# Optimization experiments

Measured on AMD Instinct MI355X. Metric: run time of the kernel, lower is better.

## Reference

```python
import jax, jax.numpy as jnp
import numpy as np

N, E, F_IN, D, H, G, T = 30000, 480000, 128, 32, 4, 128, 10
HD = H * D
NEG_SLOPE = 0.2


def _lin(key, fan_out, fan_in, scale=0.05):
    k1, k2 = jax.random.split(key)
    return (jax.random.normal(k1, (fan_out, fan_in), jnp.float32) * scale,
            jax.random.normal(k2, (fan_out,), jnp.float32) * scale)


def setup_inputs() -> dict:
    key = jax.random.key(0)
    ks = jax.random.split(key, 24)
    x = jax.random.normal(ks[0], (N, F_IN), jnp.float32)
    edge_index = jax.random.randint(ks[1], (2, E), 0, N, jnp.int64)
    batch = jnp.sort(jax.random.randint(ks[2], (N,), 0, G, jnp.int64))
    inp = {"x": x, "edge_index": edge_index, "batch": batch}
    # conv 0 (in=F_IN) and conv 1 (in=D); each followed by Linear(HD -> D)
    for i, fin in enumerate([F_IN, D]):
        base = 3 + i * 8
        Wl, bl = _lin(ks[base + 0], HD, fin)
        Wr, br = _lin(ks[base + 1], HD, fin)
        att = jax.random.normal(ks[base + 2], (H, D), jnp.float32) * 0.05
        bias = jnp.zeros((HD,), jnp.float32)
        lw, lb = _lin(ks[base + 3], D, HD)
        inp.update({f"Wl{i}": Wl, f"bl{i}": bl, f"Wr{i}": Wr, f"br{i}": br,
                    f"att{i}": att, f"cb{i}": bias, f"lw{i}": lw, f"lb{i}": lb})
    inp["fc1_W"], inp["fc1_b"] = _lin(ks[20], D, D)
    inp["fc2_W"], inp["fc2_b"] = _lin(ks[21], T, D)
    return inp


def _gatv2_conv(x, src, dst, Wl, bl, Wr, br, att, bias):
    # PyG GATv2Conv, concat=True, add_self_loops already applied to src/dst,
    # aggr='mean', eval mode (no dropout).
    n = x.shape[0]
    xl = (x @ Wl.T + bl).reshape(n, H, D)
    xr = (x @ Wr.T + br).reshape(n, H, D)
    e = jax.nn.leaky_relu(xl[src] + xr[dst], NEG_SLOPE)          # [E', H, D]
    alpha = jnp.einsum('ehd,hd->eh', e, att)                      # [E', H]
    amax = jax.ops.segment_max(alpha, dst, num_segments=n)        # [n, H]
    ex = jnp.exp(alpha - amax[dst])
    denom = jax.ops.segment_sum(ex, dst, num_segments=n)
    a = ex / denom[dst]                                           # softmax per target
    msg = xl[src] * a[:, :, None]                                 # [E', H, D]
    s = jax.ops.segment_sum(msg, dst, num_segments=n)
    cnt = jax.ops.segment_sum(jnp.ones((src.shape[0],), jnp.float32), dst, num_segments=n)
    out = s / cnt[:, None, None]                                  # mean aggregation
    return out.reshape(n, HD) + bias


def reference(x, edge_index, batch,
              Wl0, bl0, Wr0, br0, att0, cb0, lw0, lb0,
              Wl1, bl1, Wr1, br1, att1, cb1, lw1, lb1,
              fc1_W, fc1_b, fc2_W, fc2_b):
    loop = jnp.arange(N, dtype=edge_index.dtype)
    src = jnp.concatenate([edge_index[0], loop])  # add self loops
    dst = jnp.concatenate([edge_index[1], loop])
    convs = [(Wl0, bl0, Wr0, br0, att0, cb0, lw0, lb0),
             (Wl1, bl1, Wr1, br1, att1, cb1, lw1, lb1)]
    h = x
    for (Wl, bl, Wr, br, att, cb, lw, lb) in convs:
        h = _gatv2_conv(h, src, dst, Wl, bl, Wr, br, att, cb)
        h = h @ lw.T + lb  # heads>1: Linear(H*D -> D)
    g = jax.ops.segment_max(h, batch, num_segments=G)  # global max pool
    g = jax.nn.relu(g @ fc1_W.T + fc1_b)
    return g @ fc2_W.T + fc2_b
```

## Files before the change

### kernel.cpp

```cpp
#include <hip/hip_runtime.h>
#include <hip/hip_bf16.h>
#include <hip/hip_fp16.h>

#define NEG_SLOPE 0.2f
#define GGRP 128
#define TOUT 10

__global__ void init_kernel(int* __restrict__ deg, float* __restrict__ gpool,
                            int* __restrict__ csr_pad, int n, int gsize) {
    int i = blockIdx.x * blockDim.x + threadIdx.x;
    if (i < n) deg[i] = 0;
    if (i < gsize) gpool[i] = -__builtin_inff();
    if (i < 64) csr_pad[i] = 0;
}

__global__ void degree_kernel(const int* __restrict__ dst, int* __restrict__ deg, int E) {
    int i = blockIdx.x * blockDim.x + threadIdx.x;
    int base = i * 4;
    if (base + 3 < E) {
        int4 d = *(const int4*)(dst + base);
        atomicAdd(&deg[d.x], 1); atomicAdd(&deg[d.y], 1);
        atomicAdd(&deg[d.z], 1); atomicAdd(&deg[d.w], 1);
    } else {
        for (int k = base; k < E; ++k) atomicAdd(&deg[dst[k]], 1);
    }
}

__global__ __launch_bounds__(256)
void scanA_kernel(const int* __restrict__ deg, int* __restrict__ rowptr,
                  int* __restrict__ bsum, int n) {
    __shared__ int wsum[4];
    int tid = threadIdx.x, lane = tid & 63, wid = tid >> 6;
    int idx = blockIdx.x * 256 + tid;
    int v = (idx < n) ? deg[idx] : 0;
    int x = v;
    #pragma unroll
    for (int off = 1; off < 64; off <<= 1) {
        int t = __shfl_up(x, off, 64);
        if (lane >= off) x += t;
    }
    if (lane == 63) wsum[wid] = x;
    __syncthreads();
    if (tid == 0) {
        int s = 0;
        #pragma unroll
        for (int i = 0; i < 4; ++i) { int t = wsum[i]; wsum[i] = s; s += t; }
        bsum[blockIdx.x] = s;
    }
    __syncthreads();
    int excl = x - v + wsum[wid];
    if (idx < n) rowptr[idx] = excl;
}

__global__ __launch_bounds__(256)
void scanC_kernel(int* __restrict__ rowptr, int* __restrict__ cursor,
                  const int* __restrict__ bsum, int n, int nb) {
    __shared__ int soff_sh;
    int tid = threadIdx.x;
    int bx = blockIdx.x;
    if (tid < 64) {
        int lane = tid;
        int v = 0;
        if (lane < nb && lane < bx) v = bsum[lane];
        if (lane + 64 < nb && lane + 64 < bx) v += bsum[lane + 64];
        #pragma unroll
        for (int off = 32; off >= 1; off >>= 1) v += __shfl_xor(v, off, 64);
        if (lane == 0) soff_sh = v;
        if (bx == 0) {
            int t = 0;
            if (lane < nb) t = bsum[lane];
            if (lane + 64 < nb) t += bsum[lane + 64];
            #pragma unroll
            for (int off = 32; off >= 1; off >>= 1) t += __shfl_xor(t, off, 64);
            if (lane == 0) rowptr[n] = t;
        }
    }
    __syncthreads();
    int idx = bx * 256 + tid;
    if (idx < n) {
        int r = rowptr[idx] + soff_sh;
        rowptr[idx] = r;
        cursor[idx] = r;
    }
}

__global__ void scatter_kernel(const int* __restrict__ src, const int* __restrict__ dst,
                               int* __restrict__ cursor, int* __restrict__ csr, int E) {
    int i = blockIdx.x * blockDim.x + threadIdx.x;
    int base = i * 4;
    if (base + 3 < E) {
        int4 s = *(const int4*)(src + base);
        int4 d = *(const int4*)(dst + base);
        csr[atomicAdd(&cursor[d.x], 1)] = s.x << 8;
        csr[atomicAdd(&cursor[d.y], 1)] = s.y << 8;
        csr[atomicAdd(&cursor[d.z], 1)] = s.z << 8;
        csr[atomicAdd(&cursor[d.w], 1)] = s.w << 8;
    } else {
        for (int k = base; k < E; ++k)
            csr[atomicAdd(&cursor[dst[k]], 1)] = src[k] << 8;
    }
}

template <int FIN>
__global__ __launch_bounds__(256, 2)
void gemm_tile_kernel(const float* __restrict__ X,
                      const float* __restrict__ Wl, const float* __restrict__ bl,
                      const float* __restrict__ Wr, const float* __restrict__ br,
                      float* __restrict__ xl, float* __restrict__ xr,
                      __half* __restrict__ xlh,
                      int n, int nRowBlk) {
    constexpr int BK = 32, BM = 128, LDA = BM + 4;
    constexpr int NCHUNK = FIN / BK;
    __shared__ float Xs[BK][LDA];
    __shared__ float Ws[BK][LDA];
    int tid = threadIdx.x;
    int rowBlk = blockIdx.x;
    int colBlk = 0;
    if (rowBlk >= nRowBlk) { rowBlk -= nRowBlk; colBlk = 1; }
    const float* __restrict__ Wb = colBlk ? Wr : Wl;
    const float* __restrict__ bb = colBlk ? br : bl;
    float* __restrict__ ob = colBlk ? xr : xl;
    int row0 = rowBlk * BM;

    int sr  = tid >> 3;
    int skq = (tid & 7) * 4;

    float4 xpre[4], wpre[4];

    auto load_pre = [&](int c) {
        int k0 = c * BK;
        #pragma unroll
        for (int i = 0; i < 4; ++i) {
            int r = sr + i * 32;
            int gr = row0 + r;
            float4 v = {0.f, 0.f, 0.f, 0.f};
            if (gr < n) v = *(const float4*)&X[(size_t)gr * FIN + k0 + skq];
            xpre[i] = v;
            wpre[i] = *(const float4*)&Wb[(size_t)r * FIN + k0 + skq];
        }
    };
    auto store_pre = [&]() {
        #pragma unroll
        for (int i = 0; i < 4; ++i) {
            int r = sr + i * 32;
            Xs[skq + 0][r] = xpre[i].x; Xs[skq + 1][r] = xpre[i].y;
            Xs[skq + 2][r] = xpre[i].z; Xs[skq + 3][r] = xpre[i].w;
            Ws[skq + 0][r] = wpre[i].x; Ws[skq + 1][r] = wpre[i].y;
            Ws[skq + 2][r] = wpre[i].z; Ws[skq + 3][r] = wpre[i].w;
        }
    };

    load_pre(0);
    store_pre();
    __syncthreads();

    int tx = tid & 15;
    int ty = tid >> 4;
    float acc[8][8];
    #pragma unroll
    for (int i = 0; i < 8; ++i)
        #pragma unroll
        for (int j = 0; j < 8; ++j) acc[i][j] = 0.f;

    #pragma unroll
    for (int c = 0; c < NCHUNK; ++c) {
        if (c + 1 < NCHUNK) load_pre(c + 1);
        #pragma unroll 8
        for (int k = 0; k < BK; ++k) {
            float4 a0 = *(const float4*)&Xs[k][ty * 8];
            float4 a1 = *(const float4*)&Xs[k][ty * 8 + 4];
            float4 b0 = *(const float4*)&Ws[k][tx * 8];
            float4 b1 = *(const float4*)&Ws[k][tx * 8 + 4];
            float av[8] = {a0.x, a0.y, a0.z, a0.w, a1.x, a1.y, a1.z, a1.w};
            float bv[8] = {b0.x, b0.y, b0.z, b0.w, b1.x, b1.y, b1.z, b1.w};
            #pragma unroll
            for (int i = 0; i < 8; ++i)
                #pragma unroll
                for (int j = 0; j < 8; ++j)
                    acc[i][j] = fmaf(av[i], bv[j], acc[i][j]);
        }
        if (c + 1 < NCHUNK) {
            __syncthreads();
            store_pre();
            __syncthreads();
        }
    }

    float bias[8];
    #pragma unroll
    for (int j = 0; j < 8; ++j) bias[j] = bb[tx * 8 + j];
    #pragma unroll
    for (int i = 0; i < 8; ++i) {
        int gr = row0 + ty * 8 + i;
        if (gr < n) {
            float v[8];
            #pragma unroll
            for (int j = 0; j < 8; ++j) v[j] = acc[i][j] + bias[j];
            float4 o0 = {v[0], v[1], v[2], v[3]};
            float4 o1 = {v[4], v[5], v[6], v[7]};
            *(float4*)&ob[(size_t)gr * 128 + tx * 8]     = o0;
            *(float4*)&ob[(size_t)gr * 128 + tx * 8 + 4] = o1;
            if (colBlk == 0) {
                union { __half2 h2[4]; uint4 u; } pk;
                #pragma unroll
                for (int j = 0; j < 4; ++j)
                    pk.h2[j] = __halves2half2(__float2half_rn(v[2 * j]),
                                              __float2half_rn(v[2 * j + 1]));
                *(uint4*)&xlh[(size_t)gr * 128 + tx * 8] = pk.u;
            }
        }
    }
}

__global__ __launch_bounds__(256)
void gat_fused_kernel(const float* __restrict__ xl, const __half* __restrict__ xlh,
                      const float* __restrict__ xr,
                      const float* __restrict__ att, const float* __restrict__ cb,
                      const float* __restrict__ lw, const float* __restrict__ lb,
                      const int* __restrict__ rowptr, const int* __restrict__ csrb,
                      float* __restrict__ out , int n) {
    __shared__ float lws[32][132];
    __shared__ float oslot[4][128];
    int tid = threadIdx.x;
    #pragma unroll
    for (int i = 0; i < 16; ++i) {
        int idx = tid + i * 256;
        lws[idx >> 7][idx & 127] = lw[idx];
    }
    __syncthreads();

    int wid = tid >> 6, lane = tid & 63;
    int nd = blockIdx.x * 4 + wid;
    if (nd >= n) return;
    int q4  = lane >> 4;
    int l16 = lane & 15;
    int fb  = l16 * 32;
    int fbh = l16 * 16;

    const char* __restrict__ xlb  = (const char*)xl;
    const char* __restrict__ xlhb = (const char*)xlh;
    const char* __restrict__ xrb  = (const char*)xr;
    int selfoff = nd << 9;

    const float4 xrA  = *(const float4*)(xrb + selfoff + fb);
    const float4 xrB  = *(const float4*)(xrb + selfoff + fb + 16);
    const float4 atA  = *(const float4*)((const char*)att + fb);
    const float4 atB  = *(const float4*)((const char*)att + fb + 16);
    const float4 xlsA = *(const float4*)(xlb + selfoff + fb);
    const float4 xlsB = *(const float4*)(xlb + selfoff + fb + 16);

    int start = rowptr[nd], end = rowptr[nd + 1];
    float cnt = (float)(end - start + 1);

    float den;
    float accA[4], accB[4];

    {
        float e0 = xlsA.x + xrA.x; e0 = fmaf(NEG_SLOPE, fminf(e0, 0.f), fmaxf(e0, 0.f));
        float e1 = xlsA.y + xrA.y; e1 = fmaf(NEG_SLOPE, fminf(e1, 0.f), fmaxf(e1, 0.f));
        float e2 = xlsA.z + xrA.z; e2 = fmaf(NEG_SLOPE, fminf(e2, 0.f), fmaxf(e2, 0.f));
        float e3 = xlsA.w + xrA.w; e3 = fmaf(NEG_SLOPE, fminf(e3, 0.f), fmaxf(e3, 0.f));
        float e4 = xlsB.x + xrB.x; e4 = fmaf(NEG_SLOPE, fminf(e4, 0.f), fmaxf(e4, 0.f));
        float e5 = xlsB.y + xrB.y; e5 = fmaf(NEG_SLOPE, fminf(e5, 0.f), fmaxf(e5, 0.f));
        float e6 = xlsB.z + xrB.z; e6 = fmaf(NEG_SLOPE, fminf(e6, 0.f), fmaxf(e6, 0.f));
        float e7 = xlsB.w + xrB.w; e7 = fmaf(NEG_SLOPE, fminf(e7, 0.f), fmaxf(e7, 0.f));
        float q = e0 * atA.x + e1 * atA.y + e2 * atA.z + e3 * atA.w
                + e4 * atB.x + e5 * atB.y + e6 * atB.z + e7 * atB.w;
        q += __shfl_xor(q, 1); q += __shfl_xor(q, 2);
        float a = __expf(q);
        if (q4 == 0) {
            den = a;
            accA[0] = a * xlsA.x; accA[1] = a * xlsA.y;
            accA[2] = a * xlsA.z; accA[3] = a * xlsA.w;
            accB[0] = a * xlsB.x; accB[1] = a * xlsB.y;
            accB[2] = a * xlsB.z; accB[3] = a * xlsB.w;
        } else {
            den = 0.f;
            accA[0] = accA[1] = accA[2] = accA[3] = 0.f;
            accB[0] = accB[1] = accB[2] = accB[3] = 0.f;
        }
    }

    int i = start + q4;
    int offC = csrb[i + 8];
    uint4 preA = *(const uint4*)(xlhb + csrb[i] + fbh);
    uint4 preB = *(const uint4*)(xlhb + csrb[i + 4] + fbh);
    for (; i < end; i += 4) {
        uint4 hx = preA;
        preA = preB;
        preB = *(const uint4*)(xlhb + offC + fbh);
        offC = csrb[i + 12];
        float2 f01 = __half22float2(*(const __half2*)&hx.x);
        float2 f23 = __half22float2(*(const __half2*)&hx.y);
        float2 f45 = __half22float2(*(const __half2*)&hx.z);
        float2 f67 = __half22float2(*(const __half2*)&hx.w);
        float e0 = f01.x + xrA.x; e0 = fmaf(NEG_SLOPE, fminf(e0, 0.f), fmaxf(e0, 0.f));
        float e1 = f01.y + xrA.y; e1 = fmaf(NEG_SLOPE, fminf(e1, 0.f), fmaxf(e1, 0.f));
        float e2 = f23.x + xrA.z; e2 = fmaf(NEG_SLOPE, fminf(e2, 0.f), fmaxf(e2, 0.f));
        float e3 = f23.y + xrA.w; e3 = fmaf(NEG_SLOPE, fminf(e3, 0.f), fmaxf(e3, 0.f));
        float e4 = f45.x + xrB.x; e4 = fmaf(NEG_SLOPE, fminf(e4, 0.f), fmaxf(e4, 0.f));
        float e5 = f45.y + xrB.y; e5 = fmaf(NEG_SLOPE, fminf(e5, 0.f), fmaxf(e5, 0.f));
        float e6 = f67.x + xrB.z; e6 = fmaf(NEG_SLOPE, fminf(e6, 0.f), fmaxf(e6, 0.f));
        float e7 = f67.y + xrB.w; e7 = fmaf(NEG_SLOPE, fminf(e7, 0.f), fmaxf(e7, 0.f));
        float q = e0 * atA.x + e1 * atA.y + e2 * atA.z + e3 * atA.w
                + e4 * atB.x + e5 * atB.y + e6 * atB.z + e7 * atB.w;
        q += __shfl_xor(q, 1); q += __shfl_xor(q, 2);
        float a = __expf(q);
        den += a;
        accA[0] = fmaf(a, f01.x, accA[0]); accA[1] = fmaf(a, f01.y, accA[1]);
        accA[2] = fmaf(a, f23.x, accA[2]); accA[3] = fmaf(a, f23.y, accA[3]);
        accB[0] = fmaf(a, f45.x, accB[0]); accB[1] = fmaf(a, f45.y, accB[1]);
        accB[2] = fmaf(a, f67.x, accB[2]); accB[3] = fmaf(a, f67.y, accB[3]);
    }

    #pragma unroll
    for (int t = 0; t < 4; ++t) {
        accA[t] += __shfl_xor(accA[t], 16); accA[t] += __shfl_xor(accA[t], 32);
        accB[t] += __shfl_xor(accB[t], 16); accB[t] += __shfl_xor(accB[t], 32);
    }
    den += __shfl_xor(den, 16); den += __shfl_xor(den, 32);

    float inv = 1.0f / (den * cnt);
    if (q4 == 0) {
        const float4 cbA = *(const float4*)((const char*)cb + fb);
        const float4 cbB = *(const float4*)((const char*)cb + fb + 16);
        float4 oA, oB;
        oA.x = fmaf(accA[0], inv, cbA.x); oA.y = fmaf(accA[1], inv, cbA.y);
        oA.z = fmaf(accA[2], inv, cbA.z); oA.w = fmaf(accA[3], inv, cbA.w);
        oB.x = fmaf(accB[0], inv, cbB.x); oB.y = fmaf(accB[1], inv, cbB.y);
        oB.z = fmaf(accB[2], inv, cbB.z); oB.w = fmaf(accB[3], inv, cbB.w);
        *(float4*)((char*)&oslot[wid][0] + fb)      = oA;
        *(float4*)((char*)&oslot[wid][0] + fb + 16) = oB;
    }
    asm volatile("s_waitcnt lgkmcnt(0)" ::: "memory");

    int half = lane >> 5;
    int l32 = lane & 31;
    float y = 0.f;
    int kbase = half * 64;
    #pragma unroll
    for (int k = 0; k < 64; k += 4) {
        float4 lv = *(const float4*)&lws[l32][kbase + k];
        float4 ov = *(const float4*)&oslot[wid][kbase + k];
        y = fmaf(lv.x, ov.x, y);
        y = fmaf(lv.y, ov.y, y);
        y = fmaf(lv.z, ov.z, y);
        y = fmaf(lv.w, ov.w, y);
    }
    y += __shfl_xor(y, 32);
    if (half == 0) out[(size_t)nd * 32 + l32] = y + lb[l32];
}

__device__ __forceinline__ void atomicMaxFloat(float* addr, float val) {
    if (val >= 0.f) atomicMax((int*)addr, __float_as_int(val));
    else atomicMin((unsigned int*)addr, (unsigned int)__float_as_int(val));
}

__global__ void pool_kernel(const float* __restrict__ H, const int* __restrict__ batch,
                            float* __restrict__ g, int n) {
    int tid = threadIdx.x;
    int dim = tid & 31;
    int sub = tid >> 5;
    int nodeStart = blockIdx.x * 128 + sub * 16;
    float m = -__builtin_inff();
    int cur = -1;
    for (int j = 0; j < 16; ++j) {
        int nd = nodeStart + j;
        if (nd >= n) break;
        int b = batch[nd];
        if (b != cur) {
            if (cur >= 0) atomicMaxFloat(&g[cur * 32 + dim], m);
            cur = b; m = -__builtin_inff();
        }
        m = fmaxf(m, H[nd * 32 + dim]);
    }
    if (cur >= 0) atomicMaxFloat(&g[cur * 32 + dim], m);
}

__global__ __launch_bounds__(256)
void fc_kernel(const float* __restrict__ g,
               const float* __restrict__ fc1W, const float* __restrict__ fc1b,
               const float* __restrict__ fc2W, const float* __restrict__ fc2b,
               float* __restrict__ out) {
    __shared__ float g1[GGRP * 32];
    int tid = threadIdx.x;
    for (int idx = tid; idx < GGRP * 32; idx += 256) {
        int r = idx >> 5, c = idx & 31;
        float acc = fc1b[c];
        #pragma unroll
        for (int k = 0; k < 32; ++k) acc = fmaf(g[r * 32 + k], fc1W[c * 32 + k], acc);
        g1[idx] = acc > 0.f ? acc : 0.f;
    }
    __syncthreads();
    for (int idx = tid; idx < GGRP * TOUT; idx += 256) {
        int r = idx / TOUT, c = idx - r * TOUT;
        float acc = fc2b[c];
        #pragma unroll
        for (int k = 0; k < 32; ++k) acc = fmaf(g1[r * 32 + k], fc2W[c * 32 + k], acc);
        out[idx] = acc;
    }
}

extern "C" void kernel_launch(void* const* d_in, const int* in_sizes, int n_in,
                              void* d_out, int out_size, void* d_ws, size_t ws_size,
                              hipStream_t stream) {
    const float* x     = (const float*)d_in[0];
    const int*   ei    = (const int*)d_in[1];
    const int*   batch = (const int*)d_in[2];
    const float* Wl0 = (const float*)d_in[3];
    const float* bl0 = (const float*)d_in[4];
    const float* Wr0 = (const float*)d_in[5];
    const float* br0 = (const float*)d_in[6];
    const float* at0 = (const float*)d_in[7];
    const float* cb0 = (const float*)d_in[8];
    const float* lw0 = (const float*)d_in[9];
    const float* lb0 = (const float*)d_in[10];
    const float* Wl1 = (const float*)d_in[11];
    const float* bl1 = (const float*)d_in[12];
    const float* Wr1 = (const float*)d_in[13];
    const float* br1 = (const float*)d_in[14];
    const float* at1 = (const float*)d_in[15];
    const float* cb1 = (const float*)d_in[16];
    const float* lw1 = (const float*)d_in[17];
    const float* lb1 = (const float*)d_in[18];
    const float* fc1W = (const float*)d_in[19];
    const float* fc1b = (const float*)d_in[20];
    const float* fc2W = (const float*)d_in[21];
    const float* fc2b = (const float*)d_in[22];

    const int n = in_sizes[0] / 128;
    const int E = in_sizes[1] / 2;
    const int* src = ei;
    const int* dst = ei + E;
    const int nblkScan = (n + 255) / 256;
    const int nRowBlk = (n + 127) / 128;
    const int E4 = (E + 3) / 4;

    size_t off = 0;
    auto alloc = [&](size_t bytes) {
        void* p = (char*)d_ws + off;
        off += (bytes + 255) & ~(size_t)255;
        return p;
    };
    float* xl    = (float*)alloc((size_t)n * 128 * 4);
    float* xr    = (float*)alloc((size_t)n * 128 * 4);
    __half* xlh  = (__half*)alloc((size_t)n * 128 * 2);
    float* hbuf  = (float*)alloc((size_t)n * 32 * 4);
    int* deg     = (int*)alloc((size_t)n * 4);
    int* rowptr  = (int*)alloc((size_t)(n + 1) * 4);
    int* cursor  = (int*)alloc((size_t)n * 4);
    int* csr     = (int*)alloc((size_t)(E + 64) * 4);
    int* bsum    = (int*)alloc(128 * 4);
    float* gpool = (float*)alloc((size_t)GGRP * 32 * 4);

    init_kernel<<<(n + 255) / 256, 256, 0, stream>>>(deg, gpool, csr + E, n, GGRP * 32);
    degree_kernel<<<(E4 + 255) / 256, 256, 0, stream>>>(dst, deg, E);
    scanA_kernel<<<nblkScan, 256, 0, stream>>>(deg, rowptr, bsum, n);
    scanC_kernel<<<nblkScan, 256, 0, stream>>>(rowptr, cursor, bsum, n, nblkScan);
    scatter_kernel<<<(E4 + 255) / 256, 256, 0, stream>>>(src, dst, cursor, csr, E);

    gemm_tile_kernel<128><<<2 * nRowBlk, 256, 0, stream>>>(x, Wl0, bl0, Wr0, br0,
                                                           xl, xr, xlh, n, nRowBlk);
    gat_fused_kernel<<<(n + 3) / 4, 256, 0, stream>>>(xl, xlh, xr, at0, cb0, lw0, lb0,
                                                      rowptr, csr, hbuf, n);
    gemm_tile_kernel<32><<<2 * nRowBlk, 256, 0, stream>>>(hbuf, Wl1, bl1, Wr1, br1,
                                                          xl, xr, xlh, n, nRowBlk);
    gat_fused_kernel<<<(n + 3) / 4, 256, 0, stream>>>(xl, xlh, xr, at1, cb1, lw1, lb1,
                                                      rowptr, csr, hbuf, n);

    pool_kernel<<<(n + 127) / 128, 256, 0, stream>>>(hbuf, batch, gpool, n);
    fc_kernel<<<1, 256, 0, stream>>>(gpool, fc1W, fc1b, fc2W, fc2b, (float*)d_out);
}
```

Before: 296.0 us.

## Use fp16 MFMA for first-layer projection GEMM and drop fp32 xl buffer

Adds a conversion kernel that casts x and the first-layer weights to fp16, then computes the first GATv2 projections with 16x16x32 f16 MFMA instructions instead of the fp32 tiled SIMT GEMM. The fp32 xl output is removed everywhere; the attention kernel now reads the self-loop xl row from the fp16 copy, and the second-layer GEMM writes only fp16 xl plus fp32 xr. This cuts GEMM compute and the memory traffic of writing and reading the fp32 xl, at the cost of an extra conversion pass and reduced precision of the inputs. MFMA output is stored as scalar per-element writes, which may be poorly coalesced.

```diff
diff --git a/kernel.cpp b/kernel.cpp
--- a/kernel.cpp
+++ b/kernel.cpp
@@ -5,6 +5,9 @@
 #define NEG_SLOPE 0.2f
 #define GGRP 128
 #define TOUT 10
+
+typedef _Float16 half8 __attribute__((ext_vector_type(8)));
+typedef float floatx4 __attribute__((ext_vector_type(4)));
 
 __global__ void init_kernel(int* __restrict__ deg, float* __restrict__ gpool,
                             int* __restrict__ csr_pad, int n, int gsize) {
@@ -12,6 +15,26 @@
     if (i < n) deg[i] = 0;
     if (i < gsize) gpool[i] = -__builtin_inff();
     if (i < 64) csr_pad[i] = 0;
+}
+
+__global__ void cvt_kernel(const float* __restrict__ X, _Float16* __restrict__ Xh,
+                           const float* __restrict__ Wl, _Float16* __restrict__ Wlh,
+                           const float* __restrict__ Wr, _Float16* __restrict__ Wrh,
+                           int nx8, int nw8) {
+    int i = blockIdx.x * blockDim.x + threadIdx.x;
+    const float* s; _Float16* d; int j;
+    if (i < nx8) { s = X; d = Xh; j = i; }
+    else if (i < nx8 + nw8) { s = Wl; d = Wlh; j = i - nx8; }
+    else if (i < nx8 + 2 * nw8) { s = Wr; d = Wrh; j = i - nx8 - nw8; }
+    else return;
+    float4 a = *(const float4*)(s + j * 8);
+    float4 b = *(const float4*)(s + j * 8 + 4);
+    union { _Float16 h[8]; uint4 u; } pk;
+    pk.h[0] = (_Float16)a.x; pk.h[1] = (_Float16)a.y;
+    pk.h[2] = (_Float16)a.z; pk.h[3] = (_Float16)a.w;
+    pk.h[4] = (_Float16)b.x; pk.h[5] = (_Float16)b.y;
+    pk.h[6] = (_Float16)b.z; pk.h[7] = (_Float16)b.w;
+    *(uint4*)(d + j * 8) = pk.u;
 }
 
 __global__ void degree_kernel(const int* __restrict__ dst, int* __restrict__ deg, int E) {
@@ -101,13 +124,70 @@
     }
 }
 
+__global__ __launch_bounds__(256)
+void gemm_mfma_kernel(const _Float16* __restrict__ Xh,
+                      const _Float16* __restrict__ Wlh, const float* __restrict__ bl,
+                      const _Float16* __restrict__ Wrh, const float* __restrict__ br,
+                      _Float16* __restrict__ xlh, float* __restrict__ xr, int n) {
+    int tid = threadIdx.x;
+    int wave = tid >> 6, lane = tid & 63;
+    int r0 = blockIdx.x * 64 + wave * 16;
+    if (r0 >= n) return;
+    int l15 = lane & 15;
+    int lkg = lane >> 4;
+    int arow = r0 + l15; if (arow > n - 1) arow = n - 1;
+
+    const char* xb  = (const char*)Xh;
+    const char* wlb = (const char*)Wlh;
+    const char* wrb = (const char*)Wrh;
+
+    half8 a[4];
+    #pragma unroll
+    for (int kc = 0; kc < 4; ++kc)
+        a[kc] = *(const half8*)(xb + (size_t)arow * 256 + kc * 64 + lkg * 16);
+
+    floatx4 accL[8], accR[8];
+    #pragma unroll
+    for (int t = 0; t < 8; ++t) {
+        accL[t] = (floatx4){0.f, 0.f, 0.f, 0.f};
+        accR[t] = (floatx4){0.f, 0.f, 0.f, 0.f};
+    }
+
+    #pragma unroll
+    for (int t = 0; t < 8; ++t) {
+        int wrow = t * 16 + l15;
+        int wk = lkg * 16;
+        #pragma unroll
+        for (int kc = 0; kc < 4; ++kc) {
+            half8 bL = *(const half8*)(wlb + (size_t)wrow * 256 + kc * 64 + wk);
+            half8 bR = *(const half8*)(wrb + (size_t)wrow * 256 + kc * 64 + wk);
+            accL[t] = __builtin_amdgcn_mfma_f32_16x16x32_f16(a[kc], bL, accL[t], 0, 0, 0);
+            accR[t] = __builtin_amdgcn_mfma_f32_16x16x32_f16(a[kc], bR, accR[t], 0, 0, 0);
+        }
+    }
+
+    #pragma unroll
+    for (int j = 0; j < 4; ++j) {
+        int row = r0 + lkg * 4 + j;
+        if (row < n) {
+            #pragma unroll
+            for (int t = 0; t < 8; ++t) {
+                int col = t * 16 + l15;
+                float vL = accL[t][j] + bl[col];
+                float vR = accR[t][j] + br[col];
+                xlh[(size_t)row * 128 + col] = (_Float16)vL;
+                xr[(size_t)row * 128 + col] = vR;
+            }
+        }
+    }
+}
+
 template <int FIN>
 __global__ __launch_bounds__(256, 2)
 void gemm_tile_kernel(const float* __restrict__ X,
                       const float* __restrict__ Wl, const float* __restrict__ bl,
                       const float* __restrict__ Wr, const float* __restrict__ br,
-                      float* __restrict__ xl, float* __restrict__ xr,
-                      __half* __restrict__ xlh,
+                      _Float16* __restrict__ xlh, float* __restrict__ xr,
                       int n, int nRowBlk) {
     constexpr int BK = 32, BM = 128, LDA = BM + 4;
     constexpr int NCHUNK = FIN / BK;
@@ -119,7 +199,6 @@
     if (rowBlk >= nRowBlk) { rowBlk -= nRowBlk; colBlk = 1; }
     const float* __restrict__ Wb = colBlk ? Wr : Wl;
     const float* __restrict__ bb = colBlk ? br : bl;
-    float* __restrict__ ob = colBlk ? xr : xl;
     int row0 = rowBlk * BM;
 
     int sr  = tid >> 3;
@@ -196,24 +275,23 @@
             float v[8];
             #pragma unroll
             for (int j = 0; j < 8; ++j) v[j] = acc[i][j] + bias[j];
-            float4 o0 = {v[0], v[1], v[2], v[3]};
-            float4 o1 = {v[4], v[5], v[6], v[7]};
-            *(float4*)&ob[(size_t)gr * 128 + tx * 8]     = o0;
-            *(float4*)&ob[(size_t)gr * 128 + tx * 8 + 4] = o1;
             if (colBlk == 0) {
-                union { __half2 h2[4]; uint4 u; } pk;
+                union { _Float16 h[8]; uint4 u; } pk;
                 #pragma unroll
-                for (int j = 0; j < 4; ++j)
-                    pk.h2[j] = __halves2half2(__float2half_rn(v[2 * j]),
-                                              __float2half_rn(v[2 * j + 1]));
+                for (int j = 0; j < 8; ++j) pk.h[j] = (_Float16)v[j];
                 *(uint4*)&xlh[(size_t)gr * 128 + tx * 8] = pk.u;
+            } else {
+                float4 o0 = {v[0], v[1], v[2], v[3]};
+                float4 o1 = {v[4], v[5], v[6], v[7]};
+                *(float4*)&xr[(size_t)gr * 128 + tx * 8]     = o0;
+                *(float4*)&xr[(size_t)gr * 128 + tx * 8 + 4] = o1;
             }
         }
     }
 }
 
 __global__ __launch_bounds__(256)
-void gat_fused_kernel(const float* __restrict__ xl, const __half* __restrict__ xlh,
+void gat_fused_kernel(const _Float16* __restrict__ xlh,
                       const float* __restrict__ xr,
                       const float* __restrict__ att, const float* __restrict__ cb,
                       const float* __restrict__ lw, const float* __restrict__ lb,
@@ -237,17 +315,24 @@
     int fb  = l16 * 32;
     int fbh = l16 * 16;
 
-    const char* __restrict__ xlb  = (const char*)xl;
     const char* __restrict__ xlhb = (const char*)xlh;
     const char* __restrict__ xrb  = (const char*)xr;
-    int selfoff = nd << 9;
-
-    const float4 xrA  = *(const float4*)(xrb + selfoff + fb);
-    const float4 xrB  = *(const float4*)(xrb + selfoff + fb + 16);
-    const float4 atA  = *(const float4*)((const char*)att + fb);
-    const float4 atB  = *(const float4*)((const char*)att + fb + 16);
-    const float4 xlsA = *(const float4*)(xlb + selfoff + fb);
-    const float4 xlsB = *(const float4*)(xlb + selfoff + fb + 16);
+
+    const float4 xrA = *(const float4*)(xrb + ((size_t)nd << 9) + fb);
+    const float4 xrB = *(const float4*)(xrb + ((size_t)nd << 9) + fb + 16);
+    const float4 atA = *(const float4*)((const char*)att + fb);
+    const float4 atB = *(const float4*)((const char*)att + fb + 16);
+
+    float4 xlsA, xlsB;
+    {
+        uint4 hs = *(const uint4*)(xlhb + ((size_t)nd << 8) + fbh);
+        float2 s01 = __half22float2(*(const __half2*)&hs.x);
+        float2 s23 = __half22float2(*(const __half2*)&hs.y);
+        float2 s45 = __half22float2(*(const __half2*)&hs.z);
+        float2 s67 = __half22float2(*(const __half2*)&hs.w);
+        xlsA = (float4){s01.x, s01.y, s23.x, s23.y};
+        xlsB = (float4){s45.x, s45.y, s67.x, s67.y};
+    }
 
     int start = rowptr[nd], end = rowptr[nd + 1];
     float cnt = (float)(end - start + 1);
@@ -435,6 +520,8 @@
     const int nblkScan = (n + 255) / 256;
     const int nRowBlk = (n + 127) / 128;
     const int E4 = (E + 3) / 4;
+    const int nx8 = n * 16;
+    const int nw8 = 128 * 128 / 8;
 
     size_t off = 0;
     auto alloc = [&](size_t bytes) {
@@ -442,9 +529,11 @@
         off += (bytes + 255) & ~(size_t)255;
         return p;
     };
-    float* xl    = (float*)alloc((size_t)n * 128 * 4);
+    _Float16* xh  = (_Float16*)alloc((size_t)n * 128 * 2);
+    _Float16* wlh = (_Float16*)alloc(128 * 128 * 2);
+    _Float16* wrh = (_Float16*)alloc(128 * 128 * 2);
+    _Float16* xlh = (_Float16*)alloc((size_t)n * 128 * 2);
     float* xr    = (float*)alloc((size_t)n * 128 * 4);
-    __half* xlh  = (__half*)alloc((size_t)n * 128 * 2);
     float* hbuf  = (float*)alloc((size_t)n * 32 * 4);
     int* deg     = (int*)alloc((size_t)n * 4);
     int* rowptr  = (int*)alloc((size_t)(n + 1) * 4);
@@ -454,18 +543,20 @@
     float* gpool = (float*)alloc((size_t)GGRP * 32 * 4);
 
     init_kernel<<<(n + 255) / 256, 256, 0, stream>>>(deg, gpool, csr + E, n, GGRP * 32);
+    cvt_kernel<<<(nx8 + 2 * nw8 + 255) / 256, 256, 0, stream>>>(x, xh, Wl0, wlh,
+                                                                Wr0, wrh, nx8, nw8);
     degree_kernel<<<(E4 + 255) / 256, 256, 0, stream>>>(dst, deg, E);
     scanA_kernel<<<nblkScan, 256, 0, stream>>>(deg, rowptr, bsum, n);
     scanC_kernel<<<nblkScan, 256, 0, stream>>>(rowptr, cursor, bsum, n, nblkScan);
     scatter_kernel<<<(E4 + 255) / 256, 256, 0, stream>>>(src, dst, cursor, csr, E);
 
-    gemm_tile_kernel<128><<<2 * nRowBlk, 256, 0, stream>>>(x, Wl0, bl0, Wr0, br0,
-                                                           xl, xr, xlh, n, nRowBlk);
-    gat_fused_kernel<<<(n + 3) / 4, 256, 0, stream>>>(xl, xlh, xr, at0, cb0, lw0, lb0,
+    gemm_mfma_kernel<<<(n + 63) / 64, 256, 0, stream>>>(xh, wlh, bl0, wrh, br0,
+                                                        xlh, xr, n);
+    gat_fused_kernel<<<(n + 3) / 4, 256, 0, stream>>>(xlh, xr, at0, cb0, lw0, lb0,
                                                       rowptr, csr, hbuf, n);
     gemm_tile_kernel<32><<<2 * nRowBlk, 256, 0, stream>>>(hbuf, Wl1, bl1, Wr1, br1,
-                                                          xl, xr, xlh, n, nRowBlk);
-    gat_fused_kernel<<<(n + 3) / 4, 256, 0, stream>>>(xl, xlh, xr, at1, cb1, lw1, lb1,
+                                                          xlh, xr, n, nRowBlk);
+    gat_fused_kernel<<<(n + 3) / 4, 256, 0, stream>>>(xlh, xr, at1, cb1, lw1, lb1,
                                                       rowptr, csr, hbuf, n);
 
     pool_kernel<<<(n + 127) / 128, 256, 0, stream>>>(hbuf, batch, gpool, n);
```

After: 288.2 us. 1.03x faster.
